# Kernel tuning notes

Hardware: AMD Instinct MI355X
Metric: run time of the kernel (lower is better)

Reference implementation:

```python
import jax, jax.numpy as jnp
import numpy as np

B, T, F, H = 1024, 512, 64, 128


def setup_inputs() -> dict:
    key = jax.random.key(0)
    ks = jax.random.split(key, 9)
    s_ih = 1.0 / np.sqrt(H)
    inp = {
        "x": jax.random.normal(ks[0], (B, T, F), dtype=jnp.float32),
        # PyTorch GRU packed weights: [3H, F] and [3H, H], gate order (r, z, n)
        "W_ih": jax.random.uniform(ks[1], (3 * H, F), minval=-s_ih, maxval=s_ih, dtype=jnp.float32),
        "W_hh": jax.random.uniform(ks[2], (3 * H, H), minval=-s_ih, maxval=s_ih, dtype=jnp.float32),
        "b_ih": jax.random.uniform(ks[3], (3 * H,), minval=-s_ih, maxval=s_ih, dtype=jnp.float32),
        "b_hh": jax.random.uniform(ks[4], (3 * H,), minval=-s_ih, maxval=s_ih, dtype=jnp.float32),
        "W1": jax.random.uniform(ks[5], (32, H), minval=-1 / np.sqrt(H), maxval=1 / np.sqrt(H), dtype=jnp.float32),
        "b1": jax.random.uniform(ks[6], (32,), minval=-1 / np.sqrt(H), maxval=1 / np.sqrt(H), dtype=jnp.float32),
        "W2": jax.random.uniform(ks[7], (1, 32), minval=-1 / np.sqrt(32), maxval=1 / np.sqrt(32), dtype=jnp.float32),
        "b2": jax.random.uniform(ks[8], (1,), minval=-1 / np.sqrt(32), maxval=1 / np.sqrt(32), dtype=jnp.float32),
    }
    return inp


def _gru_last_hidden(x, W_ih, W_hh, b_ih, b_hh):
    # Precompute input-side gate pre-activations for all timesteps: [B, T, 3H]
    xg = jnp.einsum("btf,gf->btg", x, W_ih) + b_ih
    h0 = jnp.zeros((x.shape[0], W_hh.shape[1]), dtype=x.dtype)

    def step(h, xg_t):
        hg = h @ W_hh.T + b_hh  # [B, 3H]
        xr, xz, xn = jnp.split(xg_t, 3, axis=-1)
        hr, hz, hn = jnp.split(hg, 3, axis=-1)
        r = jax.nn.sigmoid(xr + hr)
        z = jax.nn.sigmoid(xz + hz)
        n = jnp.tanh(xn + r * hn)
        h_new = (1.0 - z) * n + z * h
        return h_new, None

    hT, _ = jax.lax.scan(step, h0, jnp.swapaxes(xg, 0, 1))  # scan over T
    return hT  # [B, H]


def reference(x, W_ih, W_hh, b_ih, b_hh, W1, b1, W2, b2):
    hT = _gru_last_hidden(x, W_ih, W_hh, b_ih, b_hh)
    hidden = jax.nn.relu(hT @ W1.T + b1)  # [B, 32]; dropout is identity at inference
    out = hidden @ W2.T + b2  # [B, 1]
    return out.squeeze(-1)  # [B]
```

## Files before the change

kernel.cpp:

```cpp
#include <hip/hip_runtime.h>
#include <math.h>


#define Bsz  1024
#define Tlen 512
#define Fdim 64
#define Hdim 128
#define Gdim 384
#define NB   16
#define NTHR 512
#define NBLK (Bsz / NB)

typedef __attribute__((ext_vector_type(8))) _Float16 f16x8;
typedef __attribute__((ext_vector_type(4))) _Float16 f16x4;
typedef __attribute__((ext_vector_type(2))) _Float16 f16x2;
typedef __attribute__((ext_vector_type(4))) float    f32x4;

__device__ __forceinline__ float fast_sigmoid(float v) {
    return __builtin_amdgcn_rcpf(1.f + __expf(-v));
}
__device__ __forceinline__ float fast_tanh(float v) {
    return 1.f - 2.f * __builtin_amdgcn_rcpf(__expf(2.f * v) + 1.f);
}

__global__ void
__attribute__((amdgpu_flat_work_group_size(NTHR, NTHR), amdgpu_waves_per_eu(2, 2)))
gru_mfma(const float* __restrict__ x,
         const float* __restrict__ W_ih, const float* __restrict__ W_hh,
         const float* __restrict__ b_ih, const float* __restrict__ b_hh,
         const float* __restrict__ W1, const float* __restrict__ b1,
         const float* __restrict__ W2, const float* __restrict__ b2,
         float* __restrict__ out)
{
    __shared__ __align__(16) _Float16 WH[24 * 4 * 4 * 128];
    __shared__ __align__(16) _Float16 WI[24 * 2 * 4 * 128];
    __shared__ __align__(16) _Float16 U0[6 * 4 * 16 * 8];
    __shared__ __align__(16) _Float16 U1[6 * 4 * 16 * 8];

    const int tid  = threadIdx.x;
    const int w    = tid >> 6;
    const int l    = tid & 63;
    const int q    = l >> 4;
    const int bcol = l & 15;
    const int b0   = blockIdx.x * NB;

    for (int i = tid; i < Gdim * Hdim; i += NTHR) {
        int gr = i >> 7, k = i & 127;
        int idx = (((gr >> 4) * 4 + (k >> 5)) * 4 + ((k & 31) >> 3)) * 128
                + (gr & 15) * 8 + (k & 7);
        WH[idx] = (_Float16)W_hh[i];
    }
    for (int i = tid; i < Gdim * Fdim; i += NTHR) {
        int gr = i >> 6, k = i & 63;
        int idx = (((gr >> 4) * 2 + (k >> 5)) * 4 + ((k & 31) >> 3)) * 128
                + (gr & 15) * 8 + (k & 7);
        WI[idx] = (_Float16)W_ih[i];
    }
    for (int i = tid; i < 2048; i += NTHR) U0[i] = (_Float16)0.f;
    {
        int e = tid * 2, bx_ = e >> 6, j = e & 63;
        float2 xv = *reinterpret_cast<const float2*>(
            &x[((size_t)(b0 + bx_) * Tlen + 0) * Fdim + j]);
        int kk = 128 + j;
        int idx = (((kk >> 5) * 4 + ((kk & 31) >> 3)) * 16 + bx_) * 8 + (kk & 7);
        U0[idx]     = (_Float16)xv.x;
        U0[idx + 1] = (_Float16)xv.y;
    }

    float br[4], bz[4], bnh[4], bnx[4];
    #pragma unroll
    for (int j = 0; j < 4; ++j) {
        int gr = 16 * w + q * 4 + j;
        br[j]  = b_ih[gr] + b_hh[gr];
        bz[j]  = b_ih[Hdim + gr] + b_hh[Hdim + gr];
        bnh[j] = b_hh[2 * Hdim + gr];
        bnx[j] = b_ih[2 * Hdim + gr];
    }

    float hp0 = 0.f, hp1 = 0.f, hp2 = 0.f, hp3 = 0.f;

    const int kb    = 16 * w + 4 * q;
    const int hbase = (((kb >> 5) * 4 + ((kb & 31) >> 3)) * 16 + bcol) * 8 + (kb & 7);

    const int e_x = tid * 2, bx = e_x >> 6, jx = e_x & 63;
    const int kx  = 128 + jx;
    const int xidx = (((kx >> 5) * 4 + ((kx & 31) >> 3)) * 16 + bx) * 8 + (kx & 7);
    const float* xsrc = &x[(size_t)(b0 + bx) * Tlen * Fdim + jx];

    __syncthreads();

#define WHF(gt, kt) (*reinterpret_cast<const f16x8*>(&WH[((((gt)*4+(kt))*4+q)*128) + (l&15)*8]))
#define WIF(gt, kt) (*reinterpret_cast<const f16x8*>(&WI[((((gt)*2+(kt))*4+q)*128) + (l&15)*8]))
#define MFMA(a, b, c) __builtin_amdgcn_mfma_f32_16x16x32_f16((a), (b), (c), 0, 0, 0)

    f16x8 whr0 = WHF(w, 0),      whr1 = WHF(w, 1),      whr2 = WHF(w, 2),      whr3 = WHF(w, 3);
    f16x8 whz0 = WHF(8 + w, 0),  whz1 = WHF(8 + w, 1),  whz2 = WHF(8 + w, 2),  whz3 = WHF(8 + w, 3);
    f16x8 whn0 = WHF(16 + w, 0), whn1 = WHF(16 + w, 1), whn2 = WHF(16 + w, 2), whn3 = WHF(16 + w, 3);
    f16x8 wir0 = WIF(w, 0),      wir1 = WIF(w, 1);
    f16x8 wiz0 = WIF(8 + w, 0),  wiz1 = WIF(8 + w, 1);
    f16x8 win0 = WIF(16 + w, 0), win1 = WIF(16 + w, 1);

    float2 xp = *reinterpret_cast<const float2*>(xsrc + (size_t)1 * Fdim);

    auto step = [&](const _Float16* __restrict__ Ur, _Float16* __restrict__ Uw, int t) {
        asm volatile("" : "+v"(whr0), "+v"(whr1), "+v"(whr2), "+v"(whr3),
                          "+v"(whz0), "+v"(whz1));
        asm volatile("" : "+v"(whz2), "+v"(whz3), "+v"(whn0), "+v"(whn1),
                          "+v"(whn2), "+v"(whn3));
        asm volatile("" : "+v"(wir0), "+v"(wir1), "+v"(wiz0), "+v"(wiz1),
                          "+v"(win0), "+v"(win1));

        f16x8 ub0 = *reinterpret_cast<const f16x8*>(&Ur[((0*4+q)*16 + bcol)*8]);
        f16x8 ub1 = *reinterpret_cast<const f16x8*>(&Ur[((1*4+q)*16 + bcol)*8]);
        f16x8 ub2 = *reinterpret_cast<const f16x8*>(&Ur[((2*4+q)*16 + bcol)*8]);
        f16x8 ub3 = *reinterpret_cast<const f16x8*>(&Ur[((3*4+q)*16 + bcol)*8]);
        f16x8 ub4 = *reinterpret_cast<const f16x8*>(&Ur[((4*4+q)*16 + bcol)*8]);
        f16x8 ub5 = *reinterpret_cast<const f16x8*>(&Ur[((5*4+q)*16 + bcol)*8]);

        float2 xw = xp;
        if (t + 2 < Tlen)
            xp = *reinterpret_cast<const float2*>(xsrc + (size_t)(t + 2) * Fdim);

        f32x4 cr  = {br[0],  br[1],  br[2],  br[3]};
        f32x4 cz  = {bz[0],  bz[1],  bz[2],  bz[3]};
        f32x4 cnh = {bnh[0], bnh[1], bnh[2], bnh[3]};
        f32x4 cnx = {bnx[0], bnx[1], bnx[2], bnx[3]};

        cr  = MFMA(whr0, ub0, cr);
        cz  = MFMA(whz0, ub0, cz);
        cnh = MFMA(whn0, ub0, cnh);
        cr  = MFMA(whr1, ub1, cr);
        cz  = MFMA(whz1, ub1, cz);
        cnh = MFMA(whn1, ub1, cnh);
        cr  = MFMA(whr2, ub2, cr);
        cz  = MFMA(whz2, ub2, cz);
        cnh = MFMA(whn2, ub2, cnh);
        cr  = MFMA(whr3, ub3, cr);
        cz  = MFMA(whz3, ub3, cz);
        cnh = MFMA(whn3, ub3, cnh);
        cr  = MFMA(wir0, ub4, cr);
        cz  = MFMA(wiz0, ub4, cz);
        cnx = MFMA(win0, ub4, cnx);
        cr  = MFMA(wir1, ub5, cr);
        cz  = MFMA(wiz1, ub5, cz);
        cnx = MFMA(win1, ub5, cnx);

        float r0 = fast_sigmoid(cr[0]), z0 = fast_sigmoid(cz[0]);
        float r1 = fast_sigmoid(cr[1]), z1 = fast_sigmoid(cz[1]);
        float r2 = fast_sigmoid(cr[2]), z2 = fast_sigmoid(cz[2]);
        float r3 = fast_sigmoid(cr[3]), z3 = fast_sigmoid(cz[3]);
        float n0 = fast_tanh(cnx[0] + r0 * cnh[0]);
        float n1 = fast_tanh(cnx[1] + r1 * cnh[1]);
        float n2 = fast_tanh(cnx[2] + r2 * cnh[2]);
        float n3 = fast_tanh(cnx[3] + r3 * cnh[3]);
        hp0 = (1.f - z0) * n0 + z0 * hp0;
        hp1 = (1.f - z1) * n1 + z1 * hp1;
        hp2 = (1.f - z2) * n2 + z2 * hp2;
        hp3 = (1.f - z3) * n3 + z3 * hp3;

        f16x4 hq = {(_Float16)hp0, (_Float16)hp1, (_Float16)hp2, (_Float16)hp3};
        *reinterpret_cast<f16x4*>(&Uw[hbase]) = hq;

        if (t + 1 < Tlen) {
            f16x2 xq = {(_Float16)xw.x, (_Float16)xw.y};
            *reinterpret_cast<f16x2*>(&Uw[xidx]) = xq;
        }
        __syncthreads();
    };

    #pragma unroll 1
    for (int t = 0; t < Tlen; t += 2) {
        step(U0, U1, t);
        step(U1, U0, t + 1);
    }

    {
        int m = tid & 31, b = tid >> 5;
        float acc = b1[m];
        #pragma unroll 8
        for (int k = 0; k < Hdim; ++k) {
            int ui = (((k >> 5) * 4 + ((k & 31) >> 3)) * 16 + b) * 8 + (k & 7);
            acc += W1[m * Hdim + k] * (float)U0[ui];
        }
        float v = W2[m] * fmaxf(acc, 0.f);
        v += __shfl_xor(v, 1,  32);
        v += __shfl_xor(v, 2,  32);
        v += __shfl_xor(v, 4,  32);
        v += __shfl_xor(v, 8,  32);
        v += __shfl_xor(v, 16, 32);
        if (m == 0) out[b0 + b] = v + b2[0];
    }
}

extern "C" void kernel_launch(void* const* d_in, const int* in_sizes, int n_in,
                              void* d_out, int out_size, void* d_ws, size_t ws_size,
                              hipStream_t stream)
{
    const float* x    = (const float*)d_in[0];
    const float* W_ih = (const float*)d_in[1];
    const float* W_hh = (const float*)d_in[2];
    const float* b_ih = (const float*)d_in[3];
    const float* b_hh = (const float*)d_in[4];
    const float* W1   = (const float*)d_in[5];
    const float* b1   = (const float*)d_in[6];
    const float* W2   = (const float*)d_in[7];
    const float* b2   = (const float*)d_in[8];
    float* out = (float*)d_out;

    dim3 grid(NBLK), block(NTHR);
    hipLaunchKernelGGL(gru_mfma, grid, block, 0, stream,
                       x, W_ih, W_hh, b_ih, b_hh, W1, b1, W2, b2, out);
}
```

Measured before the change: 331.3 us.

## Halve batch per block, pin GRU weights in AGPRs, simplify hidden update

```diff
diff --git a/kernel.cpp b/kernel.cpp
--- a/kernel.cpp
+++ b/kernel.cpp
@@ -7,7 +7,7 @@
 #define Fdim 64
 #define Hdim 128
 #define Gdim 384
-#define NB   16
+#define NB   8
 #define NTHR 512
 #define NBLK (Bsz / NB)
 
@@ -56,8 +56,8 @@
                 + (gr & 15) * 8 + (k & 7);
         WI[idx] = (_Float16)W_ih[i];
     }
-    for (int i = tid; i < 2048; i += NTHR) U0[i] = (_Float16)0.f;
-    {
+    for (int i = tid; i < 6 * 4 * 16 * 8; i += NTHR) { U0[i] = (_Float16)0.f; U1[i] = (_Float16)0.f; }
+    if (tid < NB * Fdim / 2) {
         int e = tid * 2, bx_ = e >> 6, j = e & 63;
         float2 xv = *reinterpret_cast<const float2*>(
             &x[((size_t)(b0 + bx_) * Tlen + 0) * Fdim + j]);
@@ -82,7 +82,8 @@
     const int kb    = 16 * w + 4 * q;
     const int hbase = (((kb >> 5) * 4 + ((kb & 31) >> 3)) * 16 + bcol) * 8 + (kb & 7);
 
-    const int e_x = tid * 2, bx = e_x >> 6, jx = e_x & 63;
+    const bool xthr = (tid < NB * Fdim / 2);
+    const int e_x = tid * 2, bx = xthr ? (e_x >> 6) : 0, jx = e_x & 63;
     const int kx  = 128 + jx;
     const int xidx = (((kx >> 5) * 4 + ((kx & 31) >> 3)) * 16 + bx) * 8 + (kx & 7);
     const float* xsrc = &x[(size_t)(b0 + bx) * Tlen * Fdim + jx];
@@ -100,15 +101,16 @@
     f16x8 wiz0 = WIF(8 + w, 0),  wiz1 = WIF(8 + w, 1);
     f16x8 win0 = WIF(16 + w, 0), win1 = WIF(16 + w, 1);
 
-    float2 xp = *reinterpret_cast<const float2*>(xsrc + (size_t)1 * Fdim);
+    float2 xp = {0.f, 0.f};
+    if (xthr) xp = *reinterpret_cast<const float2*>(xsrc + (size_t)1 * Fdim);
 
     auto step = [&](const _Float16* __restrict__ Ur, _Float16* __restrict__ Uw, int t) {
-        asm volatile("" : "+v"(whr0), "+v"(whr1), "+v"(whr2), "+v"(whr3),
-                          "+v"(whz0), "+v"(whz1));
-        asm volatile("" : "+v"(whz2), "+v"(whz3), "+v"(whn0), "+v"(whn1),
-                          "+v"(whn2), "+v"(whn3));
-        asm volatile("" : "+v"(wir0), "+v"(wir1), "+v"(wiz0), "+v"(wiz1),
-                          "+v"(win0), "+v"(win1));
+        asm volatile("" : "+a"(whr0), "+a"(whr1), "+a"(whr2), "+a"(whr3),
+                          "+a"(whz0), "+a"(whz1));
+        asm volatile("" : "+a"(whz2), "+a"(whz3), "+a"(whn0), "+a"(whn1),
+                          "+a"(whn2), "+a"(whn3));
+        asm volatile("" : "+a"(wir0), "+a"(wir1), "+a"(wiz0), "+a"(wiz1),
+                          "+a"(win0), "+a"(win1));
 
         f16x8 ub0 = *reinterpret_cast<const f16x8*>(&Ur[((0*4+q)*16 + bcol)*8]);
         f16x8 ub1 = *reinterpret_cast<const f16x8*>(&Ur[((1*4+q)*16 + bcol)*8]);
@@ -118,7 +120,7 @@
         f16x8 ub5 = *reinterpret_cast<const f16x8*>(&Ur[((5*4+q)*16 + bcol)*8]);
 
         float2 xw = xp;
-        if (t + 2 < Tlen)
+        if (xthr && t + 2 < Tlen)
             xp = *reinterpret_cast<const float2*>(xsrc + (size_t)(t + 2) * Fdim);
 
         f32x4 cr  = {br[0],  br[1],  br[2],  br[3]};
@@ -153,15 +155,15 @@
         float n1 = fast_tanh(cnx[1] + r1 * cnh[1]);
         float n2 = fast_tanh(cnx[2] + r2 * cnh[2]);
         float n3 = fast_tanh(cnx[3] + r3 * cnh[3]);
-        hp0 = (1.f - z0) * n0 + z0 * hp0;
-        hp1 = (1.f - z1) * n1 + z1 * hp1;
-        hp2 = (1.f - z2) * n2 + z2 * hp2;
-        hp3 = (1.f - z3) * n3 + z3 * hp3;
+        hp0 = n0 + z0 * (hp0 - n0);
+        hp1 = n1 + z1 * (hp1 - n1);
+        hp2 = n2 + z2 * (hp2 - n2);
+        hp3 = n3 + z3 * (hp3 - n3);
 
         f16x4 hq = {(_Float16)hp0, (_Float16)hp1, (_Float16)hp2, (_Float16)hp3};
         *reinterpret_cast<f16x4*>(&Uw[hbase]) = hq;
 
-        if (t + 1 < Tlen) {
+        if (xthr && t + 1 < Tlen) {
             f16x2 xq = {(_Float16)xw.x, (_Float16)xw.y};
             *reinterpret_cast<f16x2*>(&Uw[xidx]) = xq;
         }
@@ -174,8 +176,8 @@
         step(U1, U0, t + 1);
     }
 
-    {
-        int m = tid & 31, b = tid >> 5;
+    for (int sidx = tid; sidx < 32 * NB; sidx += NTHR) {
+        int m = sidx & 31, b = sidx >> 5;
         float acc = b1[m];
         #pragma unroll 8
         for (int k = 0; k < Hdim; ++k) {
```

Result: slower. 343.2 us (+3.6%).
